# Performance work log

Hardware: AMD Instinct MI355X
Metric: run time of the kernel (lower is better)

Reference implementation:

```python
import jax, jax.numpy as jnp
import numpy as np

TOP_K = 2


def setup_inputs() -> dict:
    key = jax.random.key(0)
    k1, k2 = jax.random.split(key)
    T, D, E = 16384, 2048, 64
    x = jax.random.normal(k1, (T, D), dtype=jnp.float32)
    W = jax.random.normal(k2, (E, D), dtype=jnp.float32) * 0.02  # gate weight [num_experts, embed_dim]
    return {"x": x, "W": W}


def reference(x, W):
    # gate: logits[t,e] = x[t,:] @ W[e,:]
    logits = jnp.einsum('td,ed->te', x, W)
    probs = jax.nn.softmax(logits, axis=-1)
    # top-k over experts (descending, matches torch.topk)
    top_k_weights, top_k_indices = jax.lax.top_k(probs, TOP_K)
    top_k_weights = top_k_weights / (jnp.sum(top_k_weights, axis=-1, keepdims=True) + 1e-9)
    return (top_k_weights, top_k_indices)
```

## Files before the change

### kernel.cpp

```cpp
#include <hip/hip_runtime.h>
#include <hip/hip_bf16.h>
#include <hip/hip_fp16.h>
#include <math.h>

#define T_TOKENS 16384
#define DDIM 2048
#define NEXP 64
#define REFINE_TAU 4e-3f
#define NCHK 16
#define NBLK (T_TOKENS / 16)

typedef _Float16 f16x8 __attribute__((ext_vector_type(8)));
typedef float f32x4 __attribute__((ext_vector_type(4)));

__device__ __forceinline__ void gload_lds16(const void* g, void* l) {
    __builtin_amdgcn_global_load_lds(
        (const __attribute__((address_space(1))) void*)g,
        (__attribute__((address_space(3))) void*)l, 16, 0, 0);
}

__global__ __launch_bounds__(256)
void prep_w(const float* __restrict__ W, _Float16* __restrict__ pw) {
    const int t  = blockIdx.x * 256 + threadIdx.x;
    const int r  = t >> 8;
    const int kc = (t & 255) * 8;
    const float* wp = &W[(size_t)r * DDIM + kc];
    const float4 a = *(const float4*)wp;
    const float4 b = *(const float4*)(wp + 4);
    const float f[8] = { a.x, a.y, a.z, a.w, b.x, b.y, b.z, b.w };
    f16x8 h;
#pragma unroll
    for (int j = 0; j < 8; ++j) h[j] = (_Float16)f[j];
    const int g = r >> 4, ks = kc >> 5;
    const int lane = (((kc >> 3) & 3) << 4) + (r & 15);
    *(f16x8*)&pw[(((size_t)g * 64 + ks) * 64 + lane) * 8] = h;
}

__device__ __forceinline__ bool better(double va, int ia, double vb, int ib) {
    return (va > vb) || (va == vb && ia < ib);
}

__device__ __forceinline__ double dot_f64_fast(const float* __restrict__ xrow,
                                               const float* __restrict__ wr, int lane) {
    float4 xa[8], wa[8];
#pragma unroll
    for (int q = 0; q < 8; ++q) {
        xa[q] = *(const float4*)&xrow[q * 256 + lane * 4];
        wa[q] = *(const float4*)&wr[q * 256 + lane * 4];
    }
    double s0 = 0.0, s1 = 0.0, s2 = 0.0, s3 = 0.0;
#pragma unroll
    for (int q = 0; q < 8; ++q) {
        s0 = fma((double)xa[q].x, (double)wa[q].x, s0);
        s1 = fma((double)xa[q].y, (double)wa[q].y, s1);
        s2 = fma((double)xa[q].z, (double)wa[q].z, s2);
        s3 = fma((double)xa[q].w, (double)wa[q].w, s3);
    }
    double sd = (s0 + s1) + (s2 + s3);
#pragma unroll
    for (int off = 32; off >= 1; off >>= 1) sd += __shfl_xor(sd, off);
    return sd;
}

#define STAGE(buf, c) do { \
    gload_lds16(xs0 + (size_t)(c) * 512, (char*)&xa[buf][0] + (4 * w)     * 512); \
    gload_lds16(xs1 + (size_t)(c) * 512, (char*)&xa[buf][0] + (4 * w + 2) * 512); \
} while (0)

#define LOADP(buf, c) do { \
    _Pragma("unroll") \
    for (int ks_ = 0; ks_ < 4; ++ks_) \
        pan[buf][ks_] = *(const f16x8*)&pw[(((size_t)w * 64 + (c) * 4 + ks_) * 64 + lane) * 8]; \
} while (0)

#define COMPUTE(buf) do { \
    _Pragma("unroll") \
    for (int ks_ = 0; ks_ < 4; ++ks_) { \
        const int col_ = ks_ * 128 + ((lane >> 4) << 5); \
        const f32x4 v0_ = *(const f32x4*)((const char*)&xa[buf][0] + rbase + ((col_)      ^ rswz)); \
        const f32x4 v1_ = *(const f32x4*)((const char*)&xa[buf][0] + rbase + ((col_ + 16) ^ rswz)); \
        f16x8 af_; \
        af_[0] = (_Float16)v0_[0]; af_[1] = (_Float16)v0_[1]; \
        af_[2] = (_Float16)v0_[2]; af_[3] = (_Float16)v0_[3]; \
        af_[4] = (_Float16)v1_[0]; af_[5] = (_Float16)v1_[1]; \
        af_[6] = (_Float16)v1_[2]; af_[7] = (_Float16)v1_[3]; \
        acc = __builtin_amdgcn_mfma_f32_16x16x32_f16(pan[buf][ks_], af_, acc, 0, 0, 0); \
    } \
} while (0)

__global__ __launch_bounds__(256)
void gate_fused(const float* __restrict__ x,
                const _Float16* __restrict__ pw,
                const float* __restrict__ W,
                float* __restrict__ out) {
    __shared__ float xa[2][2048];
    __shared__ float lg[16][68];

    const int tid  = threadIdx.x;
    const int lane = tid & 63;
    const int w    = tid >> 6;
    const int tokb = blockIdx.x * 16;

    const int r0 = 4 * w + (lane >> 5);
    const int r1 = 4 * w + 2 + (lane >> 5);
    const int v0 = ((lane & 31) * 16) ^ ((r0 & 7) << 4);
    const int v1 = ((lane & 31) * 16) ^ ((r1 & 7) << 4);
    const char* xs0 = (const char*)x + (size_t)(tokb + r0) * (DDIM * 4) + v0;
    const char* xs1 = (const char*)x + (size_t)(tokb + r1) * (DDIM * 4) + v1;

    const int rbase = (lane & 15) * 512;
    const int rswz  = (lane & 7) << 4;

    f16x8 pan[2][4];
    f32x4 acc = { 0.f, 0.f, 0.f, 0.f };

    STAGE(0, 0);
    LOADP(0, 0);
    __syncthreads();

#pragma unroll
    for (int c = 0; c < NCHK; ++c) {
        if (c + 1 < NCHK) {
            STAGE((c + 1) & 1, c + 1);
            LOADP((c + 1) & 1, c + 1);
        }
        COMPUTE(c & 1);
        __syncthreads();
    }

    *(f32x4*)&lg[lane & 15][w * 16 + ((lane >> 4) << 2)] = acc;
    __syncthreads();

    float* __restrict__ outw = out;
    float* __restrict__ outi = out + (size_t)T_TOKENS * 2;

#pragma unroll 1
    for (int t = 0; t < 4; ++t) {
        const int lt  = w * 4 + t;
        const int tok = tokb + lt;
        const float l = lg[lt][lane];

        float v1v = l; int i1 = lane;
#pragma unroll
        for (int off = 32; off >= 1; off >>= 1) {
            const float ov = __shfl_xor(v1v, off);
            const int   oi = __shfl_xor(i1, off);
            if (ov > v1v || (ov == v1v && oi < i1)) { v1v = ov; i1 = oi; }
        }
        float v2v = (lane == i1) ? -INFINITY : l; int i2 = lane;
#pragma unroll
        for (int off = 32; off >= 1; off >>= 1) {
            const float ov = __shfl_xor(v2v, off);
            const int   oi = __shfl_xor(i2, off);
            if (ov > v2v || (ov == v2v && oi < i2)) { v2v = ov; i2 = oi; }
        }
        float v3v = (lane == i1 || lane == i2) ? -INFINITY : l; int i3 = lane;
#pragma unroll
        for (int off = 32; off >= 1; off >>= 1) {
            const float ov = __shfl_xor(v3v, off);
            const int   oi = __shfl_xor(i3, off);
            if (ov > v3v || (ov == v3v && oi < i3)) { v3v = ov; i3 = oi; }
        }

        const float p = expf(l - v1v);
        float s = p;
#pragma unroll
        for (int off = 32; off >= 1; off >>= 1) s += __shfl_xor(s, off);

        int iA = i1, iB = i2;
        if ((v1v - v2v) < REFINE_TAU || (v2v - v3v) < REFINE_TAU) {
            const float* __restrict__ xrow = x + (size_t)tok * DDIM;
            double La = dot_f64_fast(xrow, W + (size_t)i1 * DDIM, lane);
            double Lb = dot_f64_fast(xrow, W + (size_t)i2 * DDIM, lane);
            double Lc = dot_f64_fast(xrow, W + (size_t)i3 * DDIM, lane);
            int ia = i1, ib = i2, ic = i3;
            if (!better(La, ia, Lb, ib)) { double tv = La; La = Lb; Lb = tv; int ti = ia; ia = ib; ib = ti; }
            if (!better(Lb, ib, Lc, ic)) { double tv = Lb; Lb = Lc; Lc = tv; int ti = ib; ib = ic; ic = ti; }
            if (!better(La, ia, Lb, ib)) { double tv = La; La = Lb; Lb = tv; int ti = ia; ia = ib; ib = ti; }
            iA = ia; iB = ib;
        }

        const float pA = __shfl(p, iA);
        const float pB = __shfl(p, iB);
        const float pa_ = pA / s;
        const float pb_ = pB / s;
        const float inv = 1.0f / (pa_ + pb_ + 1e-9f);

        if (lane == 0) {
            const size_t tg2 = (size_t)tok;
            outw[tg2 * 2]     = pa_ * inv;
            outw[tg2 * 2 + 1] = pb_ * inv;
            outi[tg2 * 2]     = (float)iA;
            outi[tg2 * 2 + 1] = (float)iB;
        }
    }
}

extern "C" void kernel_launch(void* const* d_in, const int* in_sizes, int n_in,
                              void* d_out, int out_size, void* d_ws, size_t ws_size,
                              hipStream_t stream) {
    const float* x = (const float*)d_in[0];
    const float* W = (const float*)d_in[1];
    float* out = (float*)d_out;
    _Float16* pw = (_Float16*)d_ws;

    prep_w<<<NEXP * DDIM / 8 / 256, 256, 0, stream>>>(W, pw);
    gate_fused<<<NBLK, 256, 0, stream>>>(x, pw, W, out);
}
```

Measured before the change: 45.21 us.

## Deepen x staging to four LDS buffers with explicit vmcnt-controlled pipeline

Measured after the change: 53.85 us. 19.1% more time.

```diff
diff --git a/kernel.cpp b/kernel.cpp
--- a/kernel.cpp
+++ b/kernel.cpp
@@ -62,38 +62,51 @@
     return sd;
 }
 
-#define STAGE(buf, c) do { \
-    gload_lds16(xs0 + (size_t)(c) * 512, (char*)&xa[buf][0] + (4 * w)     * 512); \
-    gload_lds16(xs1 + (size_t)(c) * 512, (char*)&xa[buf][0] + (4 * w + 2) * 512); \
-} while (0)
-
-#define LOADP(buf, c) do { \
-    _Pragma("unroll") \
-    for (int ks_ = 0; ks_ < 4; ++ks_) \
-        pan[buf][ks_] = *(const f16x8*)&pw[(((size_t)w * 64 + (c) * 4 + ks_) * 64 + lane) * 8]; \
-} while (0)
-
-#define COMPUTE(buf) do { \
+#define GLD(dst, p) asm volatile("global_load_dwordx4 %0, %1, off" \
+                                 : "=v"(dst) : "v"(p) : "memory")
+
+#define STAGE(c) do { \
+    gload_lds16(xs0 + (size_t)(c) * 512, (char*)&xa[0][0] + ((c) & 3) * 8192 + (4 * w) * 512); \
+    gload_lds16(xs1 + (size_t)(c) * 512, (char*)&xa[0][0] + ((c) & 3) * 8192 + (4 * w + 2) * 512); \
+} while (0)
+
+#define GLDP(c) do { \
+    GLD(pf[(c) & 1][0], pwp + ((size_t)(c) * 4 + 0) * 1024); \
+    GLD(pf[(c) & 1][1], pwp + ((size_t)(c) * 4 + 1) * 1024); \
+    GLD(pf[(c) & 1][2], pwp + ((size_t)(c) * 4 + 2) * 1024); \
+    GLD(pf[(c) & 1][3], pwp + ((size_t)(c) * 4 + 3) * 1024); \
+} while (0)
+
+#define WAITV(N) do { \
+    asm volatile("s_waitcnt vmcnt(" #N ")" ::: "memory"); \
+    __builtin_amdgcn_sched_barrier(0); \
+} while (0)
+
+#define COMPUTE(c) do { \
+    const char* xb_ = (const char*)&xa[0][0] + ((c) & 3) * 8192; \
     _Pragma("unroll") \
     for (int ks_ = 0; ks_ < 4; ++ks_) { \
         const int col_ = ks_ * 128 + ((lane >> 4) << 5); \
-        const f32x4 v0_ = *(const f32x4*)((const char*)&xa[buf][0] + rbase + ((col_)      ^ rswz)); \
-        const f32x4 v1_ = *(const f32x4*)((const char*)&xa[buf][0] + rbase + ((col_ + 16) ^ rswz)); \
+        const f32x4 v0_ = *(const f32x4*)(xb_ + rbase + ((col_)      ^ rswz)); \
+        const f32x4 v1_ = *(const f32x4*)(xb_ + rbase + ((col_ + 16) ^ rswz)); \
         f16x8 af_; \
         af_[0] = (_Float16)v0_[0]; af_[1] = (_Float16)v0_[1]; \
         af_[2] = (_Float16)v0_[2]; af_[3] = (_Float16)v0_[3]; \
         af_[4] = (_Float16)v1_[0]; af_[5] = (_Float16)v1_[1]; \
         af_[6] = (_Float16)v1_[2]; af_[7] = (_Float16)v1_[3]; \
-        acc = __builtin_amdgcn_mfma_f32_16x16x32_f16(pan[buf][ks_], af_, acc, 0, 0, 0); \
+        acc = __builtin_amdgcn_mfma_f32_16x16x32_f16( \
+            __builtin_bit_cast(f16x8, pf[(c) & 1][ks_]), af_, acc, 0, 0, 0); \
     } \
 } while (0)
+
+#define BAR() do { __builtin_amdgcn_s_barrier(); __builtin_amdgcn_sched_barrier(0); } while (0)
 
 __global__ __launch_bounds__(256)
 void gate_fused(const float* __restrict__ x,
                 const _Float16* __restrict__ pw,
                 const float* __restrict__ W,
                 float* __restrict__ out) {
-    __shared__ float xa[2][2048];
+    __shared__ float xa[4][2048];
     __shared__ float lg[16][68];
 
     const int tid  = threadIdx.x;
@@ -108,25 +121,33 @@
     const char* xs0 = (const char*)x + (size_t)(tokb + r0) * (DDIM * 4) + v0;
     const char* xs1 = (const char*)x + (size_t)(tokb + r1) * (DDIM * 4) + v1;
 
+    const char* pwp = (const char*)pw + (size_t)w * 65536 + (size_t)lane * 16;
+
     const int rbase = (lane & 15) * 512;
     const int rswz  = (lane & 7) << 4;
 
-    f16x8 pan[2][4];
+    float4 pf[2][4];
     f32x4 acc = { 0.f, 0.f, 0.f, 0.f };
 
-    STAGE(0, 0);
-    LOADP(0, 0);
-    __syncthreads();
-
-#pragma unroll
-    for (int c = 0; c < NCHK; ++c) {
-        if (c + 1 < NCHK) {
-            STAGE((c + 1) & 1, c + 1);
-            LOADP((c + 1) & 1, c + 1);
-        }
-        COMPUTE(c & 1);
-        __syncthreads();
-    }
+    STAGE(0); STAGE(1); STAGE(2);
+    GLDP(0);  GLDP(1);
+
+    WAITV(4); BAR(); COMPUTE(0);  BAR(); STAGE(3);  GLDP(2);
+    WAITV(6); BAR(); COMPUTE(1);  BAR(); STAGE(4);  GLDP(3);
+    WAITV(6); BAR(); COMPUTE(2);  BAR(); STAGE(5);  GLDP(4);
+    WAITV(6); BAR(); COMPUTE(3);  BAR(); STAGE(6);  GLDP(5);
+    WAITV(6); BAR(); COMPUTE(4);  BAR(); STAGE(7);  GLDP(6);
+    WAITV(6); BAR(); COMPUTE(5);  BAR(); STAGE(8);  GLDP(7);
+    WAITV(6); BAR(); COMPUTE(6);  BAR(); STAGE(9);  GLDP(8);
+    WAITV(6); BAR(); COMPUTE(7);  BAR(); STAGE(10); GLDP(9);
+    WAITV(6); BAR(); COMPUTE(8);  BAR(); STAGE(11); GLDP(10);
+    WAITV(6); BAR(); COMPUTE(9);  BAR(); STAGE(12); GLDP(11);
+    WAITV(6); BAR(); COMPUTE(10); BAR(); STAGE(13); GLDP(12);
+    WAITV(6); BAR(); COMPUTE(11); BAR(); STAGE(14); GLDP(13);
+    WAITV(6); BAR(); COMPUTE(12); BAR(); STAGE(15); GLDP(14);
+    WAITV(6); BAR(); COMPUTE(13); BAR();            GLDP(15);
+    WAITV(4); BAR(); COMPUTE(14); BAR();
+    WAITV(0); BAR(); COMPUTE(15);
 
     *(f32x4*)&lg[lane & 15][w * 16 + ((lane >> 4) << 2)] = acc;
     __syncthreads();
```
